# Kernel tuning notes

Measured on AMD Instinct MI355X. Metric: run time of the kernel, lower is better.

The kernel has to match this reference:

```python
import jax, jax.numpy as jnp
import numpy as np

T, LQ, C = 6, 300, 256
NH, NL, PC, TW, PT = 8, 4, 4, 2, 2
DFF = 1024
HD = C // NH
SHAPES = [(96, 128), (48, 64), (24, 32), (12, 16)]
LIN = sum(h * w for h, w in SHAPES)
EPS = 1e-5


def _ln(x, g, b):
    m = x.mean(-1, keepdims=True)
    v = ((x - m) ** 2).mean(-1, keepdims=True)
    return (x - m) * jax.lax.rsqrt(v + EPS) * g + b


def _bilinear(img, loc):
    # img [T, Hl, Wl, NH, HD]; loc [T, Q, NH, P, 2] (x, y), normalized [0,1],
    # grid_sample align_corners=False + zero padding convention.
    Hl, Wl = img.shape[1], img.shape[2]
    x = loc[..., 0] * Wl - 0.5
    y = loc[..., 1] * Hl - 0.5
    x0f = jnp.floor(x)
    y0f = jnp.floor(y)
    wx = x - x0f
    wy = y - y0f
    x0 = x0f.astype(jnp.int32)
    y0 = y0f.astype(jnp.int32)
    flat = img.transpose(0, 3, 1, 2, 4).reshape(img.shape[0], NH, Hl * Wl, HD)
    b = jnp.arange(img.shape[0])[:, None, None, None]
    h = jnp.arange(NH)[None, :, None, None]

    def corner(yi, xi, w):
        valid = (xi >= 0) & (xi < Wl) & (yi >= 0) & (yi < Hl)
        idx = jnp.clip(yi, 0, Hl - 1) * Wl + jnp.clip(xi, 0, Wl - 1)
        g = flat[b, h, idx.transpose(0, 2, 1, 3)]  # [T, NH, Q, P, HD]
        w = jnp.where(valid, w, 0.0).transpose(0, 2, 1, 3)
        return g * w[..., None]

    out = (corner(y0, x0, (1 - wx) * (1 - wy)) + corner(y0, x0 + 1, wx * (1 - wy))
           + corner(y0 + 1, x0, (1 - wx) * wy) + corner(y0 + 1, x0 + 1, wx * wy))
    return out.transpose(0, 2, 1, 3, 4)  # [T, Q, NH, P, HD]


def _forward(tgt, query_pos, reference_points, curr_frame_offsets,
             other_frames_temporal_offsets, src, src_padding_mask,
             in_proj_w, in_proj_b, sa_out_w, sa_out_b,
             norm1_g, norm1_b, norm2_g, norm2_b, norm3_g, norm3_b,
             value_w, value_b, soff_w, soff_b, toff_w, toff_b,
             attn_w, attn_b, cross_out_w, cross_out_b,
             lin1_w, lin1_b, lin2_w, lin2_b):
    # ---- self attention (per-frame MHA over queries) ----
    q = tgt + query_pos
    wq, wk, wv = jnp.split(in_proj_w, 3, axis=0)
    bq, bk, bv = jnp.split(in_proj_b, 3)
    qh = ((q @ wq.T + bq) * (1.0 / np.sqrt(HD))).reshape(T, LQ, NH, HD)
    kh = (q @ wk.T + bk).reshape(T, LQ, NH, HD)
    vh = (tgt @ wv.T + bv).reshape(T, LQ, NH, HD)
    att = jax.nn.softmax(jnp.einsum('bqhd,bkhd->bhqk', qh, kh), axis=-1)
    sa = jnp.einsum('bhqk,bkhd->bqhd', att, vh).reshape(T, LQ, C) @ sa_out_w.T + sa_out_b
    tgt = _ln(tgt + sa, norm2_g, norm2_b)

    # ---- temporal multi-scale deformable cross attention ----
    qc = tgt + query_pos
    value = src @ value_w.T + value_b
    value = jnp.where(src_padding_mask[..., None], 0.0, value)
    value = value.reshape(T, LIN, NH, HD)

    soff = (qc @ soff_w.T + soff_b).reshape(T, LQ, NH, NL, PC, 2)
    toff = (qc @ toff_w.T + toff_b).reshape(T, LQ, NH, NL, TW, PT, 2)
    aw = (qc @ attn_w.T + attn_b).reshape(T, LQ, NH, NL * (PC + TW * PT))
    aw = jax.nn.softmax(aw, axis=-1).reshape(T, LQ, NH, NL, PC + TW * PT)
    aw_c = aw[..., :PC]                                  # [T,LQ,NH,NL,PC]
    aw_t = aw[..., PC:].reshape(T, LQ, NH, NL, TW, PT)

    norm = jnp.array([[w, h] for h, w in SHAPES], jnp.float32)  # [NL,2] (x,y)
    ref = reference_points[:, :, None, :, None, :]       # [T,LQ,1,NL,1,2]
    cfo = curr_frame_offsets[:, :, None, :, None, :]
    loc_c = ref + cfo + soff / norm[None, None, None, :, None, :]
    ofo = other_frames_temporal_offsets.transpose(0, 1, 3, 2, 4)[:, :, None, :, :, None, :]
    loc_t = ref[:, :, :, :, None, :, :] + ofo + toff / norm[None, None, None, :, None, None, :]

    # temporal window frame indices: nearest neighbours, clipped to clip bounds
    deltas = np.array([-(i // 2 + 1) if i % 2 == 0 else (i // 2 + 1) for i in range(TW)])
    frame_idx = np.clip(np.arange(T)[:, None] + deltas[None, :], 0, T - 1)  # [T,TW]

    out = jnp.zeros((T, LQ, NH, HD), tgt.dtype)
    start = 0
    for l, (hl, wl) in enumerate(SHAPES):
        v_l = value[:, start:start + hl * wl].reshape(T, hl, wl, NH, HD)
        s = _bilinear(v_l, loc_c[:, :, :, l])            # [T,LQ,NH,PC,HD]
        out = out + (s * aw_c[:, :, :, l, :, None]).sum(3)
        for w in range(TW):
            s = _bilinear(v_l[frame_idx[:, w]], loc_t[:, :, :, l, w])
            out = out + (s * aw_t[:, :, :, l, w, :, None]).sum(3)
        start += hl * wl
    cross = out.reshape(T, LQ, C) @ cross_out_w.T + cross_out_b
    tgt = _ln(tgt + cross, norm1_g, norm1_b)

    # ---- FFN ----
    ff = jax.nn.relu(tgt @ lin1_w.T + lin1_b) @ lin2_w.T + lin2_b
    return _ln(tgt + ff, norm3_g, norm3_b)


def setup_inputs():
    ks = jax.random.split(jax.random.key(0), 24)
    r = lambda i, s: jax.random.normal(ks[i], s, jnp.float32)
    u = lambda i, s: jax.random.uniform(ks[i], s, dtype=jnp.float32)
    w = lambda i, s: r(i, s) * 0.02
    shp = np.array(SHAPES, np.int64)
    lsi = np.concatenate([[0], np.cumsum(shp[:, 0] * shp[:, 1])[:-1]])
    return {
        'tgt': r(0, (T, LQ, C)),
        'query_pos': r(1, (T, LQ, C)),
        'reference_points': u(2, (T, LQ, NL, 2)),
        'curr_frame_offsets': u(3, (T, LQ, NL, 2)) * 0.1,
        'other_frames_temporal_offsets': u(4, (T, LQ, TW, NL, 2)) * 0.1,
        'src': r(5, (T, LIN, C)),
        'src_spatial_shapes': jnp.asarray(shp),
        'level_start_index': jnp.asarray(lsi),
        'src_padding_mask': jnp.zeros((T, LIN), bool),
        'in_proj_w': w(6, (3 * C, C)), 'in_proj_b': jnp.zeros((3 * C,)),
        'sa_out_w': w(7, (C, C)), 'sa_out_b': jnp.zeros((C,)),
        'norm1_g': jnp.ones((C,)), 'norm1_b': jnp.zeros((C,)),
        'norm2_g': jnp.ones((C,)), 'norm2_b': jnp.zeros((C,)),
        'norm3_g': jnp.ones((C,)), 'norm3_b': jnp.zeros((C,)),
        'value_w': w(8, (C, C)), 'value_b': jnp.zeros((C,)),
        'soff_w': w(9, (NH * NL * PC * 2, C)), 'soff_b': jnp.zeros((NH * NL * PC * 2,)),
        'toff_w': w(10, (NH * NL * TW * PT * 2, C)), 'toff_b': jnp.zeros((NH * NL * TW * PT * 2,)),
        'attn_w': w(11, (NH * NL * (PC + TW * PT), C)), 'attn_b': jnp.zeros((NH * NL * (PC + TW * PT),)),
        'cross_out_w': w(12, (C, C)), 'cross_out_b': jnp.zeros((C,)),
        'lin1_w': w(13, (DFF, C)), 'lin1_b': jnp.zeros((DFF,)),
        'lin2_w': w(14, (C, DFF)), 'lin2_b': jnp.zeros((C,)),
    }


def reference(tgt, query_pos, reference_points, curr_frame_offsets,
              other_frames_temporal_offsets, src, src_spatial_shapes,
              level_start_index, src_padding_mask,
              in_proj_w, in_proj_b, sa_out_w, sa_out_b,
              norm1_g, norm1_b, norm2_g, norm2_b, norm3_g, norm3_b,
              value_w, value_b, soff_w, soff_b, toff_w, toff_b,
              attn_w, attn_b, cross_out_w, cross_out_b,
              lin1_w, lin1_b, lin2_w, lin2_b):
    # src_spatial_shapes / level_start_index are static (match SHAPES constants)
    return _forward(tgt, query_pos, reference_points, curr_frame_offsets,
                    other_frames_temporal_offsets, src, src_padding_mask,
                    in_proj_w, in_proj_b, sa_out_w, sa_out_b,
                    norm1_g, norm1_b, norm2_g, norm2_b, norm3_g, norm3_b,
                    value_w, value_b, soff_w, soff_b, toff_w, toff_b,
                    attn_w, attn_b, cross_out_w, cross_out_b,
                    lin1_w, lin1_b, lin2_w, lin2_b)
```

## Files before the change

### kernel.cpp

```cpp
#include <hip/hip_runtime.h>
#include <math.h>

#define T_ 6
#define LQ_ 300
#define C_ 256
#define NH_ 8
#define HD_ 32
#define NL_ 4
#define PC_ 4
#define TW_ 2
#define PT_ 2
#define DFF_ 1024
#define LIN_ 16320
#define NQ_ (T_*LQ_)

typedef unsigned int uint32;
typedef unsigned short us;

__device__ __forceinline__ float b2f(us u) {
    union { float f; unsigned i; } x; x.i = ((unsigned)u) << 16; return x.f;
}
__device__ __forceinline__ us f2b(float f) {
    union { float f; unsigned i; } x; x.f = f;
    unsigned r = x.i + 0x7fffu + ((x.i >> 16) & 1u);
    return (us)(r >> 16);
}
__device__ __forceinline__ uint32 pack2(float a, float b) {
    return (uint32)f2b(a) | ((uint32)f2b(b) << 16);
}

typedef __bf16 bf16x8 __attribute__((ext_vector_type(8)));
typedef float  f32x4  __attribute__((ext_vector_type(4)));

__global__ void add_f32(const float4* __restrict__ a, const float4* __restrict__ b,
                        float4* __restrict__ o, int n4) {
    int i = blockIdx.x * 256 + threadIdx.x;
    if (i < n4) {
        float4 x = a[i], y = b[i];
        o[i] = make_float4(x.x + y.x, x.y + y.y, x.z + y.z, x.w + y.w);
    }
}

template<bool RELU>
__device__ __forceinline__ void gemm64_core(
        us* As, us* Bs,
        const float* __restrict__ A, const float* __restrict__ Bw,
        const float* __restrict__ bias, float* __restrict__ Cmat,
        int ldc, int cn0, int M, int K) {
    constexpr int LDA = 40;
    int tid  = threadIdx.x;
    int wave = tid >> 6, lane = tid & 63;
    int bm = blockIdx.x * 64;
    int wm = (wave >> 1) * 32, wn = (wave & 1) * 32;

    f32x4 acc00 = {0.f,0.f,0.f,0.f}, acc01 = {0.f,0.f,0.f,0.f};
    f32x4 acc10 = {0.f,0.f,0.f,0.f}, acc11 = {0.f,0.f,0.f,0.f};

    int srow = tid >> 2, scol = (tid & 3) * 8;
    int arow = bm + srow;
    const bool aval = arow < M;
    const size_t aoff = (size_t)arow * K + scol;
    const size_t boff = (size_t)srow * K + scol;

    int fr = lane & 15, quad = lane >> 4;
    const us* pa0 = As + (wm + fr) * LDA + quad * 8;
    const us* pa1 = pa0 + 16 * LDA;
    const us* pb0 = Bs + (wn + fr) * LDA + quad * 8;
    const us* pb1 = pb0 + 16 * LDA;

    for (int k0 = 0; k0 < K; k0 += 256) {
        float4 ar[8][2], br[8][2];
        #pragma unroll
        for (int c = 0; c < 8; ++c) {
            int kk = k0 + c * 32;
            if (aval) {
                ar[c][0] = *(const float4*)(A + aoff + kk);
                ar[c][1] = *(const float4*)(A + aoff + kk + 4);
            } else {
                ar[c][0] = make_float4(0.f,0.f,0.f,0.f);
                ar[c][1] = make_float4(0.f,0.f,0.f,0.f);
            }
            br[c][0] = *(const float4*)(Bw + boff + kk);
            br[c][1] = *(const float4*)(Bw + boff + kk + 4);
        }
        #pragma unroll
        for (int c = 0; c < 8; ++c) {
            uint4 ap, bp;
            ap.x = pack2(ar[c][0].x, ar[c][0].y); ap.y = pack2(ar[c][0].z, ar[c][0].w);
            ap.z = pack2(ar[c][1].x, ar[c][1].y); ap.w = pack2(ar[c][1].z, ar[c][1].w);
            bp.x = pack2(br[c][0].x, br[c][0].y); bp.y = pack2(br[c][0].z, br[c][0].w);
            bp.z = pack2(br[c][1].x, br[c][1].y); bp.w = pack2(br[c][1].z, br[c][1].w);
            __syncthreads();
            *(uint4*)(As + srow * LDA + scol) = ap;
            *(uint4*)(Bs + srow * LDA + scol) = bp;
            __syncthreads();
            bf16x8 a0 = *(const bf16x8*)pa0;
            bf16x8 a1 = *(const bf16x8*)pa1;
            bf16x8 b0 = *(const bf16x8*)pb0;
            bf16x8 b1 = *(const bf16x8*)pb1;
            acc00 = __builtin_amdgcn_mfma_f32_16x16x32_bf16(a0, b0, acc00, 0, 0, 0);
            acc01 = __builtin_amdgcn_mfma_f32_16x16x32_bf16(a0, b1, acc01, 0, 0, 0);
            acc10 = __builtin_amdgcn_mfma_f32_16x16x32_bf16(a1, b0, acc10, 0, 0, 0);
            acc11 = __builtin_amdgcn_mfma_f32_16x16x32_bf16(a1, b1, acc11, 0, 0, 0);
        }
    }

    int n0l = wn + fr, n1l = n0l + 16;
    float bias0 = bias[n0l], bias1 = bias[n1l];
    int mbase = bm + wm + quad * 4;
    #pragma unroll
    for (int r = 0; r < 4; ++r) {
        int m0 = mbase + r, m1 = m0 + 16;
        float v00 = acc00[r] + bias0, v01 = acc01[r] + bias1;
        float v10 = acc10[r] + bias0, v11 = acc11[r] + bias1;
        if (RELU) {
            v00 = fmaxf(v00, 0.f); v01 = fmaxf(v01, 0.f);
            v10 = fmaxf(v10, 0.f); v11 = fmaxf(v11, 0.f);
        }
        if (m0 < M) {
            Cmat[(size_t)m0 * ldc + cn0 + n0l] = v00;
            Cmat[(size_t)m0 * ldc + cn0 + n1l] = v01;
        }
        if (m1 < M) {
            Cmat[(size_t)m1 * ldc + cn0 + n0l] = v10;
            Cmat[(size_t)m1 * ldc + cn0 + n1l] = v11;
        }
    }
}

template<bool RELU>
__global__ __launch_bounds__(256, 2) void gemm_std(
        const float* __restrict__ A, const float* __restrict__ W,
        const float* __restrict__ bias, float* __restrict__ C,
        int M, int N, int K) {
    __shared__ __align__(16) us As[64 * 40];
    __shared__ __align__(16) us Bs[64 * 40];
    int cn0 = blockIdx.y * 64;
    gemm64_core<RELU>(As, Bs, A, W + (size_t)cn0 * K, bias + cn0, C, N, cn0, M, K);
}

__global__ __launch_bounds__(256, 2) void gemm_qkv(
        const float* __restrict__ qin, const float* __restrict__ tgt,
        const float* __restrict__ w, const float* __restrict__ b,
        float* __restrict__ qkb, float* __restrict__ vbuf) {
    __shared__ __align__(16) us As[64 * 40];
    __shared__ __align__(16) us Bs[64 * 40];
    int y = blockIdx.y;
    const float* A; const float* W; const float* bias; float* O; int ldc, cn0;
    if (y < 8) {
        A = qin; W = w + (size_t)y * 64 * 256; bias = b + y * 64;
        O = qkb; ldc = 512; cn0 = y * 64;
    } else {
        int yy = y - 8;
        A = tgt; W = w + (size_t)(512 + yy * 64) * 256; bias = b + 512 + yy * 64;
        O = vbuf; ldc = 256; cn0 = yy * 64;
    }
    gemm64_core<false>(As, Bs, A, W, bias, O, ldc, cn0, NQ_, 256);
}

__global__ __launch_bounds__(256, 2) void gemm_proj3(
        const float* __restrict__ qc,
        const float* __restrict__ sw, const float* __restrict__ sb,
        const float* __restrict__ tw, const float* __restrict__ tb,
        const float* __restrict__ aw, const float* __restrict__ ab,
        float* __restrict__ so, float* __restrict__ to, float* __restrict__ ao) {
    __shared__ __align__(16) us As[64 * 40];
    __shared__ __align__(16) us Bs[64 * 40];
    int y = blockIdx.y, g = y >> 2, cn0 = (y & 3) * 64;
    const float* W; const float* bias; float* O;
    if (g == 0)      { W = sw; bias = sb; O = so; }
    else if (g == 1) { W = tw; bias = tb; O = to; }
    else             { W = aw; bias = ab; O = ao; }
    gemm64_core<false>(As, Bs, qc, W + (size_t)cn0 * 256, bias + cn0, O, 256, cn0, NQ_, 256);
}

__global__ __launch_bounds__(256, 2) void gemm_value(
        const float* __restrict__ src, const float* __restrict__ W,
        const float* __restrict__ bias, us* __restrict__ out) {
    constexpr int LDA = 40;
    __shared__ __align__(16) us As[64 * LDA];
    __shared__ __align__(16) us Bs[256 * LDA];
    int tid = threadIdx.x, wave = tid >> 6, lane = tid & 63;
    int bm = blockIdx.x * 64;
    int fr = lane & 15, quad = lane >> 4;
    f32x4 acc[4][4];
    #pragma unroll
    for (int i = 0; i < 4; ++i)
        #pragma unroll
        for (int j = 0; j < 4; ++j) { f32x4 z = {0.f,0.f,0.f,0.f}; acc[i][j] = z; }

    for (int k0 = 0; k0 < 256; k0 += 32) {
        float4 av[2], bv[8];
        #pragma unroll
        for (int i = 0; i < 2; ++i) {
            int f = i * 256 + tid;
            av[i] = *(const float4*)(src + (size_t)(bm + (f >> 3)) * 256 + k0 + (f & 7) * 4);
        }
        #pragma unroll
        for (int i = 0; i < 8; ++i) {
            int f = i * 256 + tid;
            bv[i] = *(const float4*)(W + (size_t)(f >> 3) * 256 + k0 + (f & 7) * 4);
        }
        __syncthreads();
        #pragma unroll
        for (int i = 0; i < 2; ++i) {
            int f = i * 256 + tid;
            uint2 p; p.x = pack2(av[i].x, av[i].y); p.y = pack2(av[i].z, av[i].w);
            *(uint2*)(As + (f >> 3) * LDA + (f & 7) * 4) = p;
        }
        #pragma unroll
        for (int i = 0; i < 8; ++i) {
            int f = i * 256 + tid;
            uint2 p; p.x = pack2(bv[i].x, bv[i].y); p.y = pack2(bv[i].z, bv[i].w);
            *(uint2*)(Bs + (f >> 3) * LDA + (f & 7) * 4) = p;
        }
        __syncthreads();
        bf16x8 af[4], bfv[4];
        #pragma unroll
        for (int mt = 0; mt < 4; ++mt)
            af[mt] = *(const bf16x8*)(As + (mt * 16 + fr) * LDA + quad * 8);
        #pragma unroll
        for (int nt = 0; nt < 4; ++nt)
            bfv[nt] = *(const bf16x8*)(Bs + (wave * 64 + nt * 16 + fr) * LDA + quad * 8);
        #pragma unroll
        for (int mt = 0; mt < 4; ++mt)
            #pragma unroll
            for (int nt = 0; nt < 4; ++nt)
                acc[mt][nt] = __builtin_amdgcn_mfma_f32_16x16x32_bf16(af[mt], bfv[nt], acc[mt][nt], 0, 0, 0);
    }
    #pragma unroll
    for (int nt = 0; nt < 4; ++nt) {
        int n = wave * 64 + nt * 16 + fr;
        float bs = bias[n];
        #pragma unroll
        for (int mt = 0; mt < 4; ++mt) {
            int mbase = bm + mt * 16 + quad * 4;
            #pragma unroll
            for (int r = 0; r < 4; ++r)
                out[(size_t)(mbase + r) * 256 + n] = f2b(acc[mt][nt][r] + bs);
        }
    }
}

__global__ __launch_bounds__(256) void attn_kernel(
        const float* __restrict__ qk, const float* __restrict__ vb,
        float* __restrict__ sain) {
    __shared__ uint32 Ksu[300 * 17];
    __shared__ uint32 Vsu[300 * 17];
    __shared__ float  Qs[32 * 32];
    __shared__ float  ps[4][304];
    int t = blockIdx.x / NH_, h = blockIdx.x % NH_;
    int q0 = blockIdx.y * 32;
    int tid = threadIdx.x;

    for (int idx = tid; idx < 300 * 16; idx += 256) {
        int row = idx >> 4, cc = idx & 15;
        float2 kv = *(const float2*)(qk + (size_t)(t * 300 + row) * 512 + 256 + h * 32 + 2 * cc);
        float2 vv = *(const float2*)(vb + (size_t)(t * 300 + row) * 256 + h * 32 + 2 * cc);
        Ksu[row * 17 + cc] = pack2(kv.x, kv.y);
        Vsu[row * 17 + cc] = pack2(vv.x, vv.y);
    }
    for (int idx = tid; idx < 1024; idx += 256) {
        int row = idx >> 5, d = idx & 31;
        int q = q0 + row;
        Qs[idx] = (q < 300) ? qk[(size_t)(t * 300 + q) * 512 + h * 32 + d] : 0.f;
    }
    __syncthreads();

    int wavei = tid >> 6, lane = tid & 63;
    const float scale = 0.17677669529663687f;

    for (int i = 0; i < 8; ++i) {
        int q = q0 + wavei * 8 + i;
        int ql = wavei * 8 + i;
        float qv[32];
        #pragma unroll
        for (int d = 0; d < 32; ++d) qv[d] = Qs[ql * 32 + d];

        float sc[5], mx = -1e30f;
        #pragma unroll
        for (int m = 0; m < 5; ++m) {
            int k = lane + 64 * m;
            float s = -1e30f;
            if (k < 300) {
                s = 0.f;
                #pragma unroll
                for (int dd = 0; dd < 16; ++dd) {
                    uint32 u = Ksu[k * 17 + dd];
                    s += qv[2 * dd]     * b2f((us)u)
                       + qv[2 * dd + 1] * b2f((us)(u >> 16));
                }
                s *= scale;
            }
            sc[m] = s; mx = fmaxf(mx, s);
        }
        #pragma unroll
        for (int off = 1; off < 64; off <<= 1) mx = fmaxf(mx, __shfl_xor(mx, off));
        float sum = 0.f;
        #pragma unroll
        for (int m = 0; m < 5; ++m) {
            int k = lane + 64 * m;
            float ev = (k < 300) ? __expf(sc[m] - mx) : 0.f;
            if (k < 300) ps[wavei][k] = ev;
            sum += ev;
        }
        #pragma unroll
        for (int off = 1; off < 64; off <<= 1) sum += __shfl_xor(sum, off);
        float inv = 1.f / sum;
        __syncthreads();

        int e16 = lane & 15, kh = lane >> 4;
        float ox = 0.f, oy = 0.f;
        int kbeg = kh * 75;
        for (int k = kbeg; k < kbeg + 75; ++k) {
            float p = ps[wavei][k];
            uint32 u = Vsu[k * 17 + e16];
            ox += p * b2f((us)u);
            oy += p * b2f((us)(u >> 16));
        }
        ox += __shfl_xor(ox, 16); ox += __shfl_xor(ox, 32);
        oy += __shfl_xor(oy, 16); oy += __shfl_xor(oy, 32);
        if (q < 300 && kh == 0) {
            *(float2*)(sain + (size_t)(t * 300 + q) * 256 + h * 32 + 2 * e16)
                = make_float2(ox * inv, oy * inv);
        }
        __syncthreads();
    }
}

__global__ __launch_bounds__(256) void sample_kernel(
        const float* __restrict__ awl,   const float* __restrict__ refp,
        const float* __restrict__ cfo,   const float* __restrict__ ofo,
        const float* __restrict__ soffo, const float* __restrict__ toffo,
        const us* __restrict__ value, float* __restrict__ samp) {
    const int HL[4] = {96, 48, 24, 12};
    const int WL[4] = {128, 64, 32, 16};
    const int ST[4] = {0, 12288, 15360, 16128};
    int b = blockIdx.x;
    int t = b / LQ_;
    int tid = threadIdx.x, h = tid >> 5, d = tid & 31;
    size_t row = (size_t)b;

    float logit = awl[row * 256 + h * 32 + d];
    float mx = logit;
    #pragma unroll
    for (int off = 16; off >= 1; off >>= 1) mx = fmaxf(mx, __shfl_xor(mx, off, 32));
    float e = __expf(logit - mx);
    float s = e;
    #pragma unroll
    for (int off = 16; off >= 1; off >>= 1) s += __shfl_xor(s, off, 32);
    float myw = e / s;

    float acc = 0.f;
    for (int smp = 0; smp < 32; ++smp) {
        int l = smp >> 3, j = smp & 7;
        float wgt = __shfl(myw, smp, 32);
        int Hl = HL[l], Wl = WL[l], st = ST[l];
        float rx = refp[(row * 4 + l) * 2 + 0];
        float ry = refp[(row * 4 + l) * 2 + 1];
        float lx, ly; int frame;
        if (j < 4) {
            lx = rx + cfo[(row * 4 + l) * 2 + 0]
               + soffo[row * 256 + h * 32 + l * 8 + j * 2 + 0] / (float)Wl;
            ly = ry + cfo[(row * 4 + l) * 2 + 1]
               + soffo[row * 256 + h * 32 + l * 8 + j * 2 + 1] / (float)Hl;
            frame = t;
        } else {
            int wi = (j - 4) >> 1, p = (j - 4) & 1;
            lx = rx + ofo[((row * 2 + wi) * 4 + l) * 2 + 0]
               + toffo[row * 256 + h * 32 + l * 8 + wi * 4 + p * 2 + 0] / (float)Wl;
            ly = ry + ofo[((row * 2 + wi) * 4 + l) * 2 + 1]
               + toffo[row * 256 + h * 32 + l * 8 + wi * 4 + p * 2 + 1] / (float)Hl;
            frame = t + (wi == 0 ? -1 : 1);
            frame = frame < 0 ? 0 : (frame > T_ - 1 ? T_ - 1 : frame);
        }
        float x = lx * (float)Wl - 0.5f, y = ly * (float)Hl - 0.5f;
        float xf = floorf(x), yf = floorf(y);
        float wx = x - xf, wy = y - yf;
        int x0 = (int)xf, y0 = (int)yf;
        float sacc = 0.f;
        size_t base = ((size_t)frame * LIN_ + st) * 256 + h * 32 + d;
        #pragma unroll
        for (int cy = 0; cy < 2; ++cy) {
            int yi = y0 + cy;
            if (yi < 0 || yi >= Hl) continue;
            float wyv = cy ? wy : 1.f - wy;
            #pragma unroll
            for (int cx = 0; cx < 2; ++cx) {
                int xi = x0 + cx;
                if (xi < 0 || xi >= Wl) continue;
                float wv = wyv * (cx ? wx : 1.f - wx);
                sacc += wv * b2f(value[base + (size_t)(yi * Wl + xi) * 256]);
            }
        }
        acc += wgt * sacc;
    }
    samp[row * 256 + h * 32 + d] = acc;
}

__global__ __launch_bounds__(256) void ln_kernel(
        const float* __restrict__ x, const float* __restrict__ y,
        const float* __restrict__ g, const float* __restrict__ bb,
        float* __restrict__ out,
        const float* __restrict__ pos, float* __restrict__ out2) {
    int row = blockIdx.x, c = threadIdx.x;
    size_t idx = (size_t)row * 256 + c;
    float v = x[idx] + y[idx];
    float s = v;
    #pragma unroll
    for (int off = 1; off < 64; off <<= 1) s += __shfl_xor(s, off);
    __shared__ float red[4];
    int wv = c >> 6;
    if ((c & 63) == 0) red[wv] = s;
    __syncthreads();
    float mean = (red[0] + red[1] + red[2] + red[3]) * (1.0f / 256.0f);
    float dv = v - mean;
    float s2 = dv * dv;
    #pragma unroll
    for (int off = 1; off < 64; off <<= 1) s2 += __shfl_xor(s2, off);
    __syncthreads();
    if ((c & 63) == 0) red[wv] = s2;
    __syncthreads();
    float var = (red[0] + red[1] + red[2] + red[3]) * (1.0f / 256.0f);
    float o = dv * rsqrtf(var + 1e-5f) * g[c] + bb[c];
    out[idx] = o;
    if (out2) out2[idx] = o + pos[idx];
}

extern "C" void kernel_launch(void* const* d_in, const int* in_sizes, int n_in,
                              void* d_out, int out_size, void* d_ws, size_t ws_size,
                              hipStream_t stream) {
    (void)in_sizes; (void)n_in; (void)out_size; (void)ws_size;
    typedef const float* cfp;
    cfp tgt   = (cfp)d_in[0];
    cfp qpos  = (cfp)d_in[1];
    cfp refp  = (cfp)d_in[2];
    cfp cfo   = (cfp)d_in[3];
    cfp ofo   = (cfp)d_in[4];
    cfp src   = (cfp)d_in[5];
    cfp in_proj_w = (cfp)d_in[9];
    cfp in_proj_b = (cfp)d_in[10];
    cfp sa_out_w  = (cfp)d_in[11];
    cfp sa_out_b  = (cfp)d_in[12];
    cfp n1g = (cfp)d_in[13], n1b = (cfp)d_in[14];
    cfp n2g = (cfp)d_in[15], n2b = (cfp)d_in[16];
    cfp n3g = (cfp)d_in[17], n3b = (cfp)d_in[18];
    cfp value_w = (cfp)d_in[19], value_b = (cfp)d_in[20];
    cfp soff_w = (cfp)d_in[21], soff_b = (cfp)d_in[22];
    cfp toff_w = (cfp)d_in[23], toff_b = (cfp)d_in[24];
    cfp attn_w = (cfp)d_in[25], attn_b = (cfp)d_in[26];
    cfp cross_w = (cfp)d_in[27], cross_b = (cfp)d_in[28];
    cfp lin1_w = (cfp)d_in[29], lin1_b = (cfp)d_in[30];
    cfp lin2_w = (cfp)d_in[31], lin2_b = (cfp)d_in[32];

    char* wp = (char*)d_ws;
    const size_t ROWB = (size_t)NQ_ * 256 * 4;
    us* value = (us*)wp;  wp += (size_t)T_ * LIN_ * 256 * 2;
    float* bigreg = (float*)wp;  wp += 4 * ROWB;
    float* qin  = bigreg;
    float* qkb  = bigreg + (size_t)NQ_ * 256;
    float* vbuf = bigreg + (size_t)NQ_ * 768;
    float* ff1  = bigreg;
    float* sain   = (float*)wp; wp += ROWB;   float* awl    = sain;
    float* sap    = (float*)wp; wp += ROWB;   float* soffo  = sap;
    float* tgt2   = (float*)wp; wp += ROWB;   float* ff2    = tgt2;
    float* qc     = (float*)wp; wp += ROWB;   float* samp   = qc;
    float* toffo  = (float*)wp; wp += ROWB;
    float* crossp = (float*)wp; wp += ROWB;
    float* tgt3   = (float*)wp; wp += ROWB;

    dim3 blk(256);
    const int mb = (NQ_ + 63) / 64;

    add_f32<<<dim3((NQ_ * 64 + 255) / 256), blk, 0, stream>>>(
        (const float4*)tgt, (const float4*)qpos, (float4*)qin, NQ_ * 64);
    gemm_qkv<<<dim3(mb, 12), blk, 0, stream>>>(qin, tgt, in_proj_w, in_proj_b, qkb, vbuf);
    attn_kernel<<<dim3(T_ * NH_, 10), blk, 0, stream>>>(qkb, vbuf, sain);
    gemm_std<false><<<dim3(mb, 4), blk, 0, stream>>>(sain, sa_out_w, sa_out_b, sap, NQ_, 256, 256);
    ln_kernel<<<dim3(NQ_), blk, 0, stream>>>(tgt, sap, n2g, n2b, tgt2, qpos, qc);
    gemm_proj3<<<dim3(mb, 12), blk, 0, stream>>>(qc, soff_w, soff_b, toff_w, toff_b,
                                                 attn_w, attn_b, soffo, toffo, awl);
    gemm_value<<<dim3((T_ * LIN_) / 64), blk, 0, stream>>>(src, value_w, value_b, value);
    sample_kernel<<<dim3(NQ_), blk, 0, stream>>>(awl, refp, cfo, ofo, soffo, toffo, value, samp);
    gemm_std<false><<<dim3(mb, 4), blk, 0, stream>>>(samp, cross_w, cross_b, crossp, NQ_, 256, 256);
    ln_kernel<<<dim3(NQ_), blk, 0, stream>>>(tgt2, crossp, n1g, n1b, tgt3, nullptr, nullptr);
    gemm_std<true><<<dim3(mb, 16), blk, 0, stream>>>(tgt3, lin1_w, lin1_b, ff1, NQ_, 1024, 256);
    gemm_std<false><<<dim3(mb, 4), blk, 0, stream>>>(ff1, lin2_w, lin2_b, ff2, NQ_, 256, 1024);
    ln_kernel<<<dim3(NQ_), blk, 0, stream>>>(tgt3, ff2, n3g, n3b, (float*)d_out, nullptr, nullptr);
}
```

Measured before the change: 404.9 us.

## Fuse query_pos add into QKV GEMM and prefetch tiles in value projection

Removes the separate elementwise add kernel by adding query_pos while the QKV GEMM loads its A operand, which saves one launch and a full write and read of the summed input. The value-projection GEMM now prefetches the next K chunk into registers while MFMAs run on the current chunk, and its launch bound asks for 3 blocks per SIMD. The bf16 pack uses the HIP intrinsic conversion instead of manual rounding. Risks are more register pressure from the prefetch under the tighter occupancy target, and an extra runtime branch on A2 inside the shared GEMM core.

After: 412.7 us. No clear change (+1.9%).

```diff
diff --git a/kernel.cpp b/kernel.cpp
--- a/kernel.cpp
+++ b/kernel.cpp
@@ -1,4 +1,5 @@
 #include <hip/hip_runtime.h>
+#include <hip/hip_bf16.h>
 #include <math.h>
 
 #define T_ 6
@@ -26,25 +27,19 @@
     return (us)(r >> 16);
 }
 __device__ __forceinline__ uint32 pack2(float a, float b) {
-    return (uint32)f2b(a) | ((uint32)f2b(b) << 16);
+    union { __hip_bfloat162 h; uint32 u; } c;
+    c.h = __float22bfloat162_rn(make_float2(a, b));
+    return c.u;
 }
 
 typedef __bf16 bf16x8 __attribute__((ext_vector_type(8)));
 typedef float  f32x4  __attribute__((ext_vector_type(4)));
-
-__global__ void add_f32(const float4* __restrict__ a, const float4* __restrict__ b,
-                        float4* __restrict__ o, int n4) {
-    int i = blockIdx.x * 256 + threadIdx.x;
-    if (i < n4) {
-        float4 x = a[i], y = b[i];
-        o[i] = make_float4(x.x + y.x, x.y + y.y, x.z + y.z, x.w + y.w);
-    }
-}
 
 template<bool RELU>
 __device__ __forceinline__ void gemm64_core(
         us* As, us* Bs,
-        const float* __restrict__ A, const float* __restrict__ Bw,
+        const float* __restrict__ A, const float* __restrict__ A2,
+        const float* __restrict__ Bw,
         const float* __restrict__ bias, float* __restrict__ Cmat,
         int ldc, int cn0, int M, int K) {
     constexpr int LDA = 40;
@@ -76,6 +71,12 @@
             if (aval) {
                 ar[c][0] = *(const float4*)(A + aoff + kk);
                 ar[c][1] = *(const float4*)(A + aoff + kk + 4);
+                if (A2) {
+                    float4 p0 = *(const float4*)(A2 + aoff + kk);
+                    float4 p1 = *(const float4*)(A2 + aoff + kk + 4);
+                    ar[c][0].x += p0.x; ar[c][0].y += p0.y; ar[c][0].z += p0.z; ar[c][0].w += p0.w;
+                    ar[c][1].x += p1.x; ar[c][1].y += p1.y; ar[c][1].z += p1.z; ar[c][1].w += p1.w;
+                }
             } else {
                 ar[c][0] = make_float4(0.f,0.f,0.f,0.f);
                 ar[c][1] = make_float4(0.f,0.f,0.f,0.f);
@@ -136,26 +137,24 @@
     __shared__ __align__(16) us As[64 * 40];
     __shared__ __align__(16) us Bs[64 * 40];
     int cn0 = blockIdx.y * 64;
-    gemm64_core<RELU>(As, Bs, A, W + (size_t)cn0 * K, bias + cn0, C, N, cn0, M, K);
+    gemm64_core<RELU>(As, Bs, A, nullptr, W + (size_t)cn0 * K, bias + cn0, C, N, cn0, M, K);
 }
 
 __global__ __launch_bounds__(256, 2) void gemm_qkv(
-        const float* __restrict__ qin, const float* __restrict__ tgt,
+        const float* __restrict__ tgt, const float* __restrict__ qpos,
         const float* __restrict__ w, const float* __restrict__ b,
         float* __restrict__ qkb, float* __restrict__ vbuf) {
     __shared__ __align__(16) us As[64 * 40];
     __shared__ __align__(16) us Bs[64 * 40];
     int y = blockIdx.y;
-    const float* A; const float* W; const float* bias; float* O; int ldc, cn0;
     if (y < 8) {
-        A = qin; W = w + (size_t)y * 64 * 256; bias = b + y * 64;
-        O = qkb; ldc = 512; cn0 = y * 64;
+        gemm64_core<false>(As, Bs, tgt, qpos, w + (size_t)y * 64 * 256, b + y * 64,
+                           qkb, 512, y * 64, NQ_, 256);
     } else {
         int yy = y - 8;
-        A = tgt; W = w + (size_t)(512 + yy * 64) * 256; bias = b + 512 + yy * 64;
-        O = vbuf; ldc = 256; cn0 = yy * 64;
-    }
-    gemm64_core<false>(As, Bs, A, W, bias, O, ldc, cn0, NQ_, 256);
+        gemm64_core<false>(As, Bs, tgt, nullptr, w + (size_t)(512 + yy * 64) * 256,
+                           b + 512 + yy * 64, vbuf, 256, yy * 64, NQ_, 256);
+    }
 }
 
 __global__ __launch_bounds__(256, 2) void gemm_proj3(
@@ -171,11 +170,11 @@
     if (g == 0)      { W = sw; bias = sb; O = so; }
     else if (g == 1) { W = tw; bias = tb; O = to; }
     else             { W = aw; bias = ab; O = ao; }
-    gemm64_core<false>(As, Bs, qc, W + (size_t)cn0 * 256, bias + cn0, O, 256, cn0, NQ_, 256);
-}
-
-__global__ __launch_bounds__(256, 2) void gemm_value(
-        const float* __restrict__ src, const float* __restrict__ W,
+    gemm64_core<false>(As, Bs, qc, nullptr, W + (size_t)cn0 * 256, bias + cn0, O, 256, cn0, NQ_, 256);
+}
+
+__global__ __launch_bounds__(256, 3) void gemm_value_pf(
+        const float* __restrict__ A, const float* __restrict__ W,
         const float* __restrict__ bias, us* __restrict__ out) {
     constexpr int LDA = 40;
     __shared__ __align__(16) us As[64 * LDA];
@@ -183,25 +182,34 @@
     int tid = threadIdx.x, wave = tid >> 6, lane = tid & 63;
     int bm = blockIdx.x * 64;
     int fr = lane & 15, quad = lane >> 4;
+
     f32x4 acc[4][4];
     #pragma unroll
     for (int i = 0; i < 4; ++i)
         #pragma unroll
         for (int j = 0; j < 4; ++j) { f32x4 z = {0.f,0.f,0.f,0.f}; acc[i][j] = z; }
 
-    for (int k0 = 0; k0 < 256; k0 += 32) {
-        float4 av[2], bv[8];
+    float4 av[2], bv[8];
+    auto ldA = [&](int c) {
+        int k0 = c * 32;
         #pragma unroll
         for (int i = 0; i < 2; ++i) {
             int f = i * 256 + tid;
-            av[i] = *(const float4*)(src + (size_t)(bm + (f >> 3)) * 256 + k0 + (f & 7) * 4);
-        }
+            av[i] = *(const float4*)(A + (size_t)(bm + (f >> 3)) * 256 + k0 + (f & 7) * 4);
+        }
+    };
+    auto ldB = [&](int c) {
+        int k0 = c * 32;
         #pragma unroll
         for (int i = 0; i < 8; ++i) {
             int f = i * 256 + tid;
             bv[i] = *(const float4*)(W + (size_t)(f >> 3) * 256 + k0 + (f & 7) * 4);
         }
-        __syncthreads();
+    };
+
+    ldA(0); ldB(0);
+    for (int c = 0; c < 8; ++c) {
+        if (c) __syncthreads();
         #pragma unroll
         for (int i = 0; i < 2; ++i) {
             int f = i * 256 + tid;
@@ -215,6 +223,7 @@
             *(uint2*)(Bs + (f >> 3) * LDA + (f & 7) * 4) = p;
         }
         __syncthreads();
+        if (c + 1 < 8) { ldA(c + 1); ldB(c + 1); }
         bf16x8 af[4], bfv[4];
         #pragma unroll
         for (int mt = 0; mt < 4; ++mt)
@@ -228,6 +237,7 @@
             for (int nt = 0; nt < 4; ++nt)
                 acc[mt][nt] = __builtin_amdgcn_mfma_f32_16x16x32_bf16(af[mt], bfv[nt], acc[mt][nt], 0, 0, 0);
     }
+
     #pragma unroll
     for (int nt = 0; nt < 4; ++nt) {
         int n = wave * 64 + nt * 16 + fr;
@@ -457,9 +467,8 @@
     const size_t ROWB = (size_t)NQ_ * 256 * 4;
     us* value = (us*)wp;  wp += (size_t)T_ * LIN_ * 256 * 2;
     float* bigreg = (float*)wp;  wp += 4 * ROWB;
-    float* qin  = bigreg;
-    float* qkb  = bigreg + (size_t)NQ_ * 256;
-    float* vbuf = bigreg + (size_t)NQ_ * 768;
+    float* qkb  = bigreg;
+    float* vbuf = bigreg + (size_t)NQ_ * 512;
     float* ff1  = bigreg;
     float* sain   = (float*)wp; wp += ROWB;   float* awl    = sain;
     float* sap    = (float*)wp; wp += ROWB;   float* soffo  = sap;
@@ -472,15 +481,13 @@
     dim3 blk(256);
     const int mb = (NQ_ + 63) / 64;
 
-    add_f32<<<dim3((NQ_ * 64 + 255) / 256), blk, 0, stream>>>(
-        (const float4*)tgt, (const float4*)qpos, (float4*)qin, NQ_ * 64);
-    gemm_qkv<<<dim3(mb, 12), blk, 0, stream>>>(qin, tgt, in_proj_w, in_proj_b, qkb, vbuf);
+    gemm_qkv<<<dim3(mb, 12), blk, 0, stream>>>(tgt, qpos, in_proj_w, in_proj_b, qkb, vbuf);
     attn_kernel<<<dim3(T_ * NH_, 10), blk, 0, stream>>>(qkb, vbuf, sain);
     gemm_std<false><<<dim3(mb, 4), blk, 0, stream>>>(sain, sa_out_w, sa_out_b, sap, NQ_, 256, 256);
     ln_kernel<<<dim3(NQ_), blk, 0, stream>>>(tgt, sap, n2g, n2b, tgt2, qpos, qc);
     gemm_proj3<<<dim3(mb, 12), blk, 0, stream>>>(qc, soff_w, soff_b, toff_w, toff_b,
                                                  attn_w, attn_b, soffo, toffo, awl);
-    gemm_value<<<dim3((T_ * LIN_) / 64), blk, 0, stream>>>(src, value_w, value_b, value);
+    gemm_value_pf<<<dim3((T_ * LIN_) / 64), blk, 0, stream>>>(src, value_w, value_b, value);
     sample_kernel<<<dim3(NQ_), blk, 0, stream>>>(awl, refp, cfo, ofo, soffo, toffo, value, samp);
     gemm_std<false><<<dim3(mb, 4), blk, 0, stream>>>(samp, cross_w, cross_b, crossp, NQ_, 256, 256);
     ln_kernel<<<dim3(NQ_), blk, 0, stream>>>(tgt2, crossp, n1g, n1b, tgt3, nullptr, nullptr);
```
